# Kernel tuning notes

Hardware: AMD Instinct MI355X
Metric: run time of the kernel (lower is better)

Reference implementation:

```python
import jax, jax.numpy as jnp
import numpy as np
from jax import lax

HEADS = 4
DIM = 64
GATE_HID = 16


def setup_inputs() -> dict:
    key = jax.random.key(0)
    ks = jax.random.split(key, 12)
    b, c, h, w = 2, DIM, 48, 48
    s = 0.05
    x = jax.random.normal(ks[0], (b, c, h, w), jnp.float32)
    Wqkv = jax.random.normal(ks[1], (3 * c, c), jnp.float32) * s
    bqkv = jax.random.normal(ks[2], (3 * c,), jnp.float32) * s
    Wpos = jax.random.normal(ks[3], (3 * c, 1, 3, 3), jnp.float32) * s
    bpos = jax.random.normal(ks[4], (3 * c,), jnp.float32) * s
    Wg1 = jax.random.normal(ks[5], (GATE_HID, 1), jnp.float32) * 0.5
    bg1 = jax.random.normal(ks[6], (GATE_HID,), jnp.float32) * 0.1
    Wg2 = jax.random.normal(ks[7], (1, GATE_HID), jnp.float32) * 0.5
    bg2 = jax.random.normal(ks[8], (1,), jnp.float32) * 0.1
    Wproj = jax.random.normal(ks[9], (c, c), jnp.float32) * s
    bproj = jax.random.normal(ks[10], (c,), jnp.float32) * s
    return {"x": x, "Wqkv": Wqkv, "bqkv": bqkv, "Wpos": Wpos, "bpos": bpos,
            "Wg1": Wg1, "bg1": bg1, "Wg2": Wg2, "bg2": bg2,
            "Wproj": Wproj, "bproj": bproj}


def _forward(x, Wqkv, bqkv, Wpos, bpos, Wg1, bg1, Wg2, bg2, Wproj, bproj):
    b, c, h, w = x.shape
    n = h * w
    heads = HEADS
    hd = c // heads
    scale = hd ** -0.5
    # qkv 1x1 conv then 3x3 depthwise positional conv
    qkv = jnp.einsum('bchw,oc->bohw', x, Wqkv) + bqkv[None, :, None, None]
    qkv = lax.conv_general_dilated(
        qkv, Wpos, window_strides=(1, 1), padding='SAME',
        feature_group_count=3 * c,
        dimension_numbers=('NCHW', 'OIHW', 'NCHW')) + bpos[None, :, None, None]
    q, k, v = jnp.split(qkv, 3, axis=1)

    def to_heads(t):
        # [b,c,h,w] -> [b,heads,n,hd]
        return t.reshape(b, c, n).transpose(0, 2, 1).reshape(b, n, heads, hd).transpose(0, 2, 1, 3)

    q, k, v = to_heads(q), to_heads(k), to_heads(v)
    attn = jnp.einsum('bhid,bhjd->bhij', q, k) * scale  # [b,heads,n,n]
    prob = jax.nn.softmax(attn, axis=-1)
    entropy = -(prob * jnp.log(jnp.clip(prob, 1e-12))).sum(-1).mean(-1)  # [b,heads]
    # entropy gate: sigmoid(fc2(relu(fc1(e)))) * 0.9 + 0.1
    hgate = jax.nn.relu(entropy[..., None] @ Wg1.T + bg1)  # [b,heads,16]
    ratio = jax.nn.sigmoid(hgate @ Wg2.T + bg2)[..., 0] * 0.9 + 0.1  # [b,heads]
    # dynamic per-(batch,head) top-k along rows via rank threshold
    keep = jnp.clip(jnp.ceil(ratio * n).astype(jnp.int32), 1, n)  # [b,heads]
    sorted_desc = -jnp.sort(-attn, axis=-1)  # [b,heads,n,n]
    idx = jnp.broadcast_to((keep - 1)[:, :, None, None], (b, heads, n, 1))
    thresh = jnp.take_along_axis(sorted_desc, idx, axis=-1)  # [b,heads,n,1]
    sparse = jnp.where(attn >= thresh, attn, -jnp.inf)
    p = jax.nn.softmax(sparse, axis=-1)
    out = jnp.einsum('bhij,bhjd->bhid', p, v)  # [b,heads,n,hd]
    out = out.transpose(0, 2, 1, 3).reshape(b, n, c)
    out = out @ Wproj.T + bproj
    return out.transpose(0, 2, 1).reshape(b, c, h, w)


def reference(x, Wqkv, bqkv, Wpos, bpos, Wg1, bg1, Wg2, bg2, Wproj, bproj):
    return _forward(x, Wqkv, bqkv, Wpos, bpos, Wg1, bg1, Wg2, bg2, Wproj, bproj)
```

## Files before the change

kernel.cpp:

```cpp
#include <hip/hip_runtime.h>
#include <hip/hip_fp16.h>


#define NEG_INF (-__builtin_huge_valf())

typedef _Float16 half8_t __attribute__((ext_vector_type(8)));
typedef float floatx4 __attribute__((ext_vector_type(4)));

__device__ __forceinline__ float key16_to_float(unsigned k) {
  unsigned short u = (k & 0x8000u) ? (unsigned short)(k & 0x7FFFu)
                                   : (unsigned short)((~k) & 0xFFFFu);
  return __half2float(__ushort_as_half(u));
}

__device__ __forceinline__ void unpack8(uint4 v, float* o) {
  float2 f0 = __half22float2(*(__half2*)&v.x);
  float2 f1 = __half22float2(*(__half2*)&v.y);
  float2 f2 = __half22float2(*(__half2*)&v.z);
  float2 f3 = __half22float2(*(__half2*)&v.w);
  o[0] = f0.x; o[1] = f0.y; o[2] = f1.x; o[3] = f1.y;
  o[4] = f2.x; o[5] = f2.y; o[6] = f3.x; o[7] = f3.y;
}

__global__ __launch_bounds__(256) void k_qkv(const float* __restrict__ x,
                                             const float* __restrict__ W,
                                             const float* __restrict__ bias,
                                             float* __restrict__ out,
                                             float* __restrict__ ent) {
  if (blockIdx.x == 0 && threadIdx.x < 8) ent[threadIdx.x] = 0.f;
  int blk = blockIdx.x;
  int chunk = blk % 9;
  int og = (blk / 9) % 48;
  int b = blk / (9 * 48);
  int o0 = og * 4;
  int pos = chunk * 256 + threadIdx.x;
  const float* xb = x + b * 64 * 2304 + pos;
  const float* w0 = W + (o0 + 0) * 64;
  const float* w1 = W + (o0 + 1) * 64;
  const float* w2 = W + (o0 + 2) * 64;
  const float* w3 = W + (o0 + 3) * 64;
  float a0 = bias[o0 + 0], a1 = bias[o0 + 1];
  float a2 = bias[o0 + 2], a3 = bias[o0 + 3];
#pragma unroll
  for (int c = 0; c < 64; c++) {
    float xv = xb[c * 2304];
    a0 = fmaf(w0[c], xv, a0);
    a1 = fmaf(w1[c], xv, a1);
    a2 = fmaf(w2[c], xv, a2);
    a3 = fmaf(w3[c], xv, a3);
  }
  out[(b * 192 + o0 + 0) * 2304 + pos] = a0;
  out[(b * 192 + o0 + 1) * 2304 + pos] = a1;
  out[(b * 192 + o0 + 2) * 2304 + pos] = a2;
  out[(b * 192 + o0 + 3) * 2304 + pos] = a3;
}

__global__ __launch_bounds__(256) void k_dw(const float* __restrict__ qkv,
                                            const float* __restrict__ Wpos,
                                            const float* __restrict__ bpos,
                                            _Float16* __restrict__ q2,
                                            _Float16* __restrict__ k2,
                                            _Float16* __restrict__ vt) {
  __shared__ float smem[16][384];
  int blk = blockIdx.x;
  int chunk = blk % 9;
  int sel = (blk / 9) % 3;
  int head = (blk / 27) % 4;
  int b = blk / 108;
  int chbase = sel * 64 + head * 16;
  int bh = b * 4 + head;
  int tid = threadIdx.x;
  int p0 = chunk * 256;
  int baserow = p0 / 48;
  int rA = min(max(baserow - 1, 0), 40);

  const float* src = qkv + (size_t)(b * 192 + chbase) * 2304;
#pragma unroll
  for (int l = 0; l < 24; l++) {
    int idx = tid + l * 256;
    int ch = idx / 384;
    int off = idx - ch * 384;
    int rr = off / 48;
    int cc = off - rr * 48;
    smem[ch][off] = src[(size_t)ch * 2304 + (rA + rr) * 48 + cc];
  }
  __syncthreads();

  int pos = p0 + tid;
  int yy = pos / 48, xx = pos - yy * 48;
  int ry = yy - rA;
  float accv[16];
#pragma unroll
  for (int d = 0; d < 16; d++) {
    const float* w = Wpos + (chbase + d) * 9;
    float a = bpos[chbase + d];
#pragma unroll
    for (int dy = -1; dy <= 1; dy++) {
      int y2 = yy + dy;
      if ((unsigned)y2 < 48u) {
#pragma unroll
        for (int dx = -1; dx <= 1; dx++) {
          int x2 = xx + dx;
          if ((unsigned)x2 < 48u)
            a = fmaf(w[(dy + 1) * 3 + (dx + 1)], smem[d][(ry + dy) * 48 + x2],
                     a);
        }
      }
    }
    accv[d] = a;
  }

  if (sel == 2) {
#pragma unroll
    for (int d = 0; d < 16; d++)
      vt[((size_t)bh * 16 + d) * 2304 + pos] = (_Float16)accv[d];
  } else {
    _Float16 h1[16], h2[16];
#pragma unroll
    for (int d = 0; d < 16; d++) {
      float a = (sel == 0) ? accv[d] * 0.25f : accv[d];
      h1[d] = (_Float16)a;
      h2[d] = (_Float16)(a - (float)h1[d]);
    }
    _Float16* dst = ((sel == 0) ? q2 : k2) + ((size_t)bh * 2304 + pos) * 32;
    uint4* d4 = (uint4*)dst;
    d4[0] = *(uint4*)&h1[0];
    d4[1] = *(uint4*)&h1[8];
    d4[2] = *(uint4*)&h2[0];
    d4[3] = *(uint4*)&h2[8];
  }
}

template <bool STORE>
__global__ __launch_bounds__(256) void k_ent_t(const _Float16* __restrict__ q2,
                                               const _Float16* __restrict__ k2,
                                               float* __restrict__ ent,
                                               _Float16* __restrict__ lgH) {
  __shared__ __align__(16) _Float16 tBuf[4][16][72];
  __shared__ float sWv[4][16], uWv[4][16];

  int blk = blockIdx.x;
  int rowtile = blk % 144;
  int bh = blk / 144;
  int row0 = rowtile * 16;
  int tid = threadIdx.x, lane = tid & 63, wave = tid >> 6;
  int m16 = lane & 15, quad = lane >> 4;

  const half8_t* q2v =
      (const half8_t*)(q2 + ((size_t)bh * 2304 + row0 + m16) * 32);
  half8_t A1 = q2v[quad];
  half8_t zh = {};
  half8_t A2 = (lane < 32) ? A1 : zh;
  const half8_t* kbase = (const half8_t*)(k2 + (size_t)bh * 2304 * 32);

  float s[4] = {0.f, 0.f, 0.f, 0.f}, u[4] = {0.f, 0.f, 0.f, 0.f};
  for (int g = 0; g < 9; g++) {
#pragma unroll
    for (int tt = 0; tt < 4; tt++) {
      int t = g * 4 + tt;
      int col = wave * 576 + t * 16 + m16;
      const half8_t* kk = kbase + (size_t)col * 4;
      half8_t b1 = kk[quad & 1];
      half8_t b2 = kk[2 + (quad & 1)];
      floatx4 acc = {};
      acc = __builtin_amdgcn_mfma_f32_16x16x32_f16(A2, b2, acc, 0, 0, 0);
      acc = __builtin_amdgcn_mfma_f32_16x16x32_f16(A1, b1, acc, 0, 0, 0);
#pragma unroll
      for (int i = 0; i < 4; i++) {
        if (STORE) tBuf[wave][quad * 4 + i][tt * 16 + m16] = (_Float16)acc[i];
        float e = __expf(acc[i]);
        s[i] += e;
        u[i] = fmaf(acc[i], e, u[i]);
      }
    }
    if (STORE) {
      __syncthreads();
      int rb = lane >> 3, seg = lane & 7;
#pragma unroll
      for (int it = 0; it < 2; it++) {
        int rr = it * 8 + rb;
        uint4 vv = *(const uint4*)&tBuf[wave][rr][seg * 8];
        *(uint4*)(lgH + ((size_t)bh * 2304 + row0 + rr) * 2304 + wave * 576 +
                  g * 64 + seg * 8) = vv;
      }
      __syncthreads();
    }
  }
#pragma unroll
  for (int off = 1; off < 16; off <<= 1) {
#pragma unroll
    for (int i = 0; i < 4; i++) {
      s[i] += __shfl_xor(s[i], off);
      u[i] += __shfl_xor(u[i], off);
    }
  }
  if (m16 == 0) {
#pragma unroll
    for (int i = 0; i < 4; i++) {
      sWv[wave][quad * 4 + i] = s[i];
      uWv[wave][quad * 4 + i] = u[i];
    }
  }
  __syncthreads();
  if (tid < 16) {
    float S = sWv[0][tid] + sWv[1][tid] + sWv[2][tid] + sWv[3][tid];
    float U = uWv[0][tid] + uWv[1][tid] + uWv[2][tid] + uWv[3][tid];
    float er = __logf(S) - U / S;
    er += __shfl_xor(er, 1);
    er += __shfl_xor(er, 2);
    er += __shfl_xor(er, 4);
    er += __shfl_xor(er, 8);
    if (tid == 0) atomicAdd(&ent[bh], er);
  }
}

template <bool CACHED>
__global__ __launch_bounds__(256, 7) void k_attn_t(
    const _Float16* __restrict__ q2, const _Float16* __restrict__ k2,
    const _Float16* __restrict__ vt, const _Float16* __restrict__ lgH,
    const float* __restrict__ ent, const float* __restrict__ Wg1,
    const float* __restrict__ bg1, const float* __restrict__ Wg2,
    const float* __restrict__ bg2, float* __restrict__ oh) {
  __shared__ __align__(16) _Float16 pbuf[4][2320];
  __shared__ float sS[4];
  __shared__ float mShF[4][4];
  __shared__ __align__(16) float redSh[4][64];

  int a = blockIdx.x;
  int v8 = a & 7;
  int idx = a >> 3;
  int q = idx & 3;
  int pi = idx >> 2;
  int bh = pi / 18;
  int rowtile = v8 + (pi % 18) * 8;
  int rowblk = rowtile * 4 + q;
  int row0 = rowblk * 4;
  int tid = threadIdx.x, lane = tid & 63, wave = tid >> 6;

  float eAvg = ent[bh] * (1.f / 2304.f);
  float gacc = bg2[0];
#pragma unroll
  for (int i = 0; i < 16; i++) {
    float h = fmaxf(fmaf(eAvg, Wg1[i], bg1[i]), 0.f);
    gacc = fmaf(h, Wg2[i], gacc);
  }
  float ratio = 0.9f / (1.f + __expf(-gacc)) + 0.1f;
  int kp = (int)ceilf(ratio * 2304.f);
  unsigned keep = (unsigned)min(max(kp, 1), 2304);

  float v[36];
  float m;
  if (CACHED) {
    const _Float16* src = lgH + ((size_t)bh * 2304 + row0 + wave) * 2304;
    const uint4* s4 = (const uint4*)src;
    float mx = NEG_INF;
#pragma unroll
    for (int it = 0; it < 4; it++) {
      uint4 r = s4[lane + it * 64];
      unpack8(r, &v[it * 8]);
    }
    {
      uint2 r2 = *(const uint2*)(src + 2048 + lane * 4);
      float2 f0 = __half22float2(*(__half2*)&r2.x);
      float2 f1 = __half22float2(*(__half2*)&r2.y);
      v[32] = f0.x; v[33] = f0.y; v[34] = f1.x; v[35] = f1.y;
    }
#pragma unroll
    for (int i = 0; i < 36; i++) mx = fmaxf(mx, v[i]);
#pragma unroll
    for (int off = 1; off < 64; off <<= 1) mx = fmaxf(mx, __shfl_xor(mx, off));
    m = mx;
  } else {
    int m16 = lane & 15, quad = lane >> 4;
    const half8_t* q2v =
        (const half8_t*)(q2 + ((size_t)bh * 2304 + row0 + (m16 & 3)) * 32);
    half8_t A1 = q2v[quad];
    half8_t zh = {};
    half8_t A2 = (lane < 32) ? A1 : zh;
    const half8_t* kbase = (const half8_t*)(k2 + (size_t)bh * 2304 * 32);
    float ml[4] = {NEG_INF, NEG_INF, NEG_INF, NEG_INF};
#pragma unroll 4
    for (int t = 0; t < 36; t++) {
      int ct = wave * 36 + t;
      int col = ct * 16 + m16;
      const half8_t* kk = kbase + (size_t)col * 4;
      half8_t b1 = kk[quad & 1];
      half8_t b2 = kk[2 + (quad & 1)];
      floatx4 acc = {};
      acc = __builtin_amdgcn_mfma_f32_16x16x32_f16(A2, b2, acc, 0, 0, 0);
      acc = __builtin_amdgcn_mfma_f32_16x16x32_f16(A1, b1, acc, 0, 0, 0);
      if (lane < 16) {
#pragma unroll
        for (int i = 0; i < 4; i++) {
          pbuf[i][ct * 16 + lane] = (_Float16)acc[i];
          ml[i] = fmaxf(ml[i], acc[i]);
        }
      }
    }
#pragma unroll
    for (int off = 1; off < 16; off <<= 1)
#pragma unroll
      for (int i = 0; i < 4; i++) ml[i] = fmaxf(ml[i], __shfl_xor(ml[i], off));
    if (lane == 0) {
#pragma unroll
      for (int i = 0; i < 4; i++) mShF[wave][i] = ml[i];
    }
    __syncthreads();
    m = fmaxf(fmaxf(mShF[0][wave], mShF[1][wave]),
              fmaxf(mShF[2][wave], mShF[3][wave]));
    const _Float16* src = pbuf[wave];
    const uint4* s4 = (const uint4*)src;
#pragma unroll
    for (int it = 0; it < 4; it++) unpack8(s4[lane + it * 64], &v[it * 8]);
    uint2 r2 = *(const uint2*)(src + 2048 + lane * 4);
    float2 f0 = __half22float2(*(__half2*)&r2.x);
    float2 f1 = __half22float2(*(__half2*)&r2.y);
    v[32] = f0.x; v[33] = f0.y; v[34] = f1.x; v[35] = f1.y;
  }

  float th;
  {
    unsigned T = 0u;
    for (int bit = 15; bit >= 0; --bit) {
      unsigned cand = T | (1u << bit);
      float cf = key16_to_float(cand);
      unsigned cnt = 0u;
#pragma unroll
      for (int i = 0; i < 36; i++)
        cnt += (unsigned)__popcll(__ballot(v[i] >= cf));
      if (cnt >= keep) {
        T = cand;
        if (cnt == keep) break;
      }
    }
    th = key16_to_float(T);
  }

  {
    float sp = 0.f;
    uint4* prow4 = (uint4*)pbuf[wave];
#pragma unroll
    for (int it = 0; it < 4; it++) {
      float p[8];
#pragma unroll
      for (int e = 0; e < 8; e++) {
        float av = v[it * 8 + e];
        p[e] = (av >= th) ? __expf(av - m) : 0.f;
        sp += p[e];
      }
      uint4 o;
      __half2 h0 = __floats2half2_rn(p[0], p[1]); o.x = *(unsigned*)&h0;
      __half2 h1 = __floats2half2_rn(p[2], p[3]); o.y = *(unsigned*)&h1;
      __half2 h2 = __floats2half2_rn(p[4], p[5]); o.z = *(unsigned*)&h2;
      __half2 h3 = __floats2half2_rn(p[6], p[7]); o.w = *(unsigned*)&h3;
      prow4[lane + it * 64] = o;
    }
    {
      float p0 = (v[32] >= th) ? __expf(v[32] - m) : 0.f;
      float p1 = (v[33] >= th) ? __expf(v[33] - m) : 0.f;
      float p2 = (v[34] >= th) ? __expf(v[34] - m) : 0.f;
      float p3 = (v[35] >= th) ? __expf(v[35] - m) : 0.f;
      sp += (p0 + p1) + (p2 + p3);
      uint2 o;
      __half2 h0 = __floats2half2_rn(p0, p1); o.x = *(unsigned*)&h0;
      __half2 h1 = __floats2half2_rn(p2, p3); o.y = *(unsigned*)&h1;
      *(uint2*)(pbuf[wave] + 2048 + lane * 4) = o;
    }
#pragma unroll
    for (int off = 1; off < 64; off <<= 1) sp += __shfl_xor(sp, off);
    if (lane == 0) sS[wave] = sp;
  }
  __syncthreads();

  {
    int m16 = lane & 15, quad = lane >> 4;
    const _Float16* vrow = vt + ((size_t)bh * 16 + m16) * 2304;
    const _Float16* prow = pbuf[m16 & 3];
    int jb0 = wave * 576 + quad * 8;
    floatx4 acc = {};
#pragma unroll 6
    for (int t = 0; t < 18; t++) {
      int jb = jb0 + t * 32;
      half8_t a2 = *(const half8_t*)&prow[jb];
      half8_t b2 = *(const half8_t*)&vrow[jb];
      acc = __builtin_amdgcn_mfma_f32_16x16x32_f16(a2, b2, acc, 0, 0, 0);
    }
    if (lane < 16) {
      *(floatx4*)&redSh[wave][m16 * 4] = acc;
    }
  }
  __syncthreads();
  if (tid < 64) {
    int r = tid & 3, d = tid >> 2;
    float s2 = redSh[0][d * 4 + r] + redSh[1][d * 4 + r] +
               redSh[2][d * 4 + r] + redSh[3][d * 4 + r];
    oh[((size_t)(bh * 2304 + row0 + r)) * 16 + d] = s2 / sS[r];
  }
}

__global__ __launch_bounds__(256) void k_proj(const float* __restrict__ oh,
                                              const float* __restrict__ Wp,
                                              const float* __restrict__ bp,
                                              float* __restrict__ out) {
  int blk = blockIdx.x;
  int chunk = blk % 9;
  int cog = (blk / 9) % 16;
  int b = blk / (9 * 16);
  int co0 = cog * 4;
  int pos = chunk * 256 + threadIdx.x;
  float a0 = bp[co0 + 0], a1 = bp[co0 + 1], a2 = bp[co0 + 2], a3 = bp[co0 + 3];
#pragma unroll
  for (int head = 0; head < 4; head++) {
    const float4* op =
        (const float4*)(oh + ((size_t)((b * 4 + head) * 2304 + pos)) * 16);
#pragma unroll
    for (int p = 0; p < 4; p++) {
      float4 o4 = op[p];
#pragma unroll
      for (int i = 0; i < 4; i++) {
        const float* wr = Wp + (co0 + i) * 64 + head * 16 + p * 4;
        float* ai = (i == 0) ? &a0 : ((i == 1) ? &a1 : ((i == 2) ? &a2 : &a3));
        *ai = fmaf(wr[0], o4.x, *ai);
        *ai = fmaf(wr[1], o4.y, *ai);
        *ai = fmaf(wr[2], o4.z, *ai);
        *ai = fmaf(wr[3], o4.w, *ai);
      }
    }
  }
  out[(b * 64 + co0 + 0) * 2304 + pos] = a0;
  out[(b * 64 + co0 + 1) * 2304 + pos] = a1;
  out[(b * 64 + co0 + 2) * 2304 + pos] = a2;
  out[(b * 64 + co0 + 3) * 2304 + pos] = a3;
}

extern "C" void kernel_launch(void* const* d_in, const int* in_sizes, int n_in,
                              void* d_out, int out_size, void* d_ws,
                              size_t ws_size, hipStream_t stream) {
  const float* x    = (const float*)d_in[0];
  const float* Wqkv = (const float*)d_in[1];
  const float* bqkv = (const float*)d_in[2];
  const float* Wpos = (const float*)d_in[3];
  const float* bpos = (const float*)d_in[4];
  const float* Wg1  = (const float*)d_in[5];
  const float* bg1  = (const float*)d_in[6];
  const float* Wg2  = (const float*)d_in[7];
  const float* bg2  = (const float*)d_in[8];
  const float* Wpr  = (const float*)d_in[9];
  const float* bpr  = (const float*)d_in[10];
  float* out = (float*)d_out;

  const size_t lgBytes = (size_t)8 * 2304 * 2304 * 2;
  const size_t baseBytes = (size_t)(884736 + 294912 + 8) * 4 +
                           (size_t)(2 * 589824 + 294912) * 2;
  bool cached = ws_size >= lgBytes + baseBytes;

  char* base = (char*)d_ws;
  _Float16* lgH = nullptr;
  if (cached) {
    lgH = (_Float16*)base;
    base += lgBytes;
  }
  float* qkv_raw = (float*)base;
  float* oh = qkv_raw + 884736;
  float* ent = oh + 294912;
  _Float16* q2 = (_Float16*)(ent + 8);
  _Float16* k2 = q2 + 589824;
  _Float16* vt = k2 + 589824;

  hipLaunchKernelGGL(k_qkv, dim3(2 * 48 * 9), dim3(256), 0, stream,
                     x, Wqkv, bqkv, qkv_raw, ent);
  hipLaunchKernelGGL(k_dw, dim3(216), dim3(256), 0, stream,
                     qkv_raw, Wpos, bpos, q2, k2, vt);
  if (cached) {
    hipLaunchKernelGGL((k_ent_t<true>), dim3(8 * 144), dim3(256), 0, stream,
                       q2, k2, ent, lgH);
    hipLaunchKernelGGL((k_attn_t<true>), dim3(8 * 576), dim3(256), 0, stream,
                       q2, k2, vt, lgH, ent, Wg1, bg1, Wg2, bg2, oh);
  } else {
    hipLaunchKernelGGL((k_ent_t<false>), dim3(8 * 144), dim3(256), 0, stream,
                       q2, k2, ent, lgH);
    hipLaunchKernelGGL((k_attn_t<false>), dim3(8 * 576), dim3(256), 0, stream,
                       q2, k2, vt, lgH, ent, Wg1, bg1, Wg2, bg2, oh);
  }
  hipLaunchKernelGGL(k_proj, dim3(2 * 16 * 9), dim3(256), 0, stream,
                     oh, Wpr, bpr, out);
}
```

Measured before the change: 199.4 us.

## Fuse output projection into attention kernel and drop softmax max subtraction

Removes the separate projection kernel. Each attention block now projects its 4 rows across all 64 output channels and atomically adds the per-head contribution into a pre-zeroed output. This removes the max computation and its reductions and stores before the exponentials, which relies on logits being small enough not to overflow exp. The depthwise conv kernel is also split into half-channel blocks to double its grid. The cost is a memset, plus atomic traffic on the output with 4-way contention per element.

```diff
diff --git a/kernel.cpp b/kernel.cpp
--- a/kernel.cpp
+++ b/kernel.cpp
@@ -61,13 +61,14 @@
                                             _Float16* __restrict__ q2,
                                             _Float16* __restrict__ k2,
                                             _Float16* __restrict__ vt) {
-  __shared__ float smem[16][384];
+  __shared__ float smem[8][384];
   int blk = blockIdx.x;
   int chunk = blk % 9;
-  int sel = (blk / 9) % 3;
-  int head = (blk / 27) % 4;
-  int b = blk / 108;
-  int chbase = sel * 64 + head * 16;
+  int half = (blk / 9) % 2;
+  int sel = (blk / 18) % 3;
+  int head = (blk / 54) % 4;
+  int b = blk / 216;
+  int chbase = sel * 64 + head * 16 + half * 8;
   int bh = b * 4 + head;
   int tid = threadIdx.x;
   int p0 = chunk * 256;
@@ -76,7 +77,7 @@
 
   const float* src = qkv + (size_t)(b * 192 + chbase) * 2304;
 #pragma unroll
-  for (int l = 0; l < 24; l++) {
+  for (int l = 0; l < 12; l++) {
     int idx = tid + l * 256;
     int ch = idx / 384;
     int off = idx - ch * 384;
@@ -89,9 +90,9 @@
   int pos = p0 + tid;
   int yy = pos / 48, xx = pos - yy * 48;
   int ry = yy - rA;
-  float accv[16];
-#pragma unroll
-  for (int d = 0; d < 16; d++) {
+  float accv[8];
+#pragma unroll
+  for (int d = 0; d < 8; d++) {
     const float* w = Wpos + (chbase + d) * 9;
     float a = bpos[chbase + d];
 #pragma unroll
@@ -112,22 +113,19 @@
 
   if (sel == 2) {
 #pragma unroll
-    for (int d = 0; d < 16; d++)
-      vt[((size_t)bh * 16 + d) * 2304 + pos] = (_Float16)accv[d];
+    for (int d = 0; d < 8; d++)
+      vt[((size_t)bh * 16 + half * 8 + d) * 2304 + pos] = (_Float16)accv[d];
   } else {
-    _Float16 h1[16], h2[16];
-#pragma unroll
-    for (int d = 0; d < 16; d++) {
+    _Float16 h1[8], h2[8];
+#pragma unroll
+    for (int d = 0; d < 8; d++) {
       float a = (sel == 0) ? accv[d] * 0.25f : accv[d];
       h1[d] = (_Float16)a;
       h2[d] = (_Float16)(a - (float)h1[d]);
     }
     _Float16* dst = ((sel == 0) ? q2 : k2) + ((size_t)bh * 2304 + pos) * 32;
-    uint4* d4 = (uint4*)dst;
-    d4[0] = *(uint4*)&h1[0];
-    d4[1] = *(uint4*)&h1[8];
-    d4[2] = *(uint4*)&h2[0];
-    d4[3] = *(uint4*)&h2[8];
+    *(uint4*)(dst + half * 8) = *(uint4*)&h1[0];
+    *(uint4*)(dst + 16 + half * 8) = *(uint4*)&h2[0];
   }
 }
 
@@ -220,11 +218,12 @@
     const _Float16* __restrict__ vt, const _Float16* __restrict__ lgH,
     const float* __restrict__ ent, const float* __restrict__ Wg1,
     const float* __restrict__ bg1, const float* __restrict__ Wg2,
-    const float* __restrict__ bg2, float* __restrict__ oh) {
+    const float* __restrict__ bg2, const float* __restrict__ Wp,
+    const float* __restrict__ bp, float* __restrict__ out) {
   __shared__ __align__(16) _Float16 pbuf[4][2320];
   __shared__ float sS[4];
-  __shared__ float mShF[4][4];
   __shared__ __align__(16) float redSh[4][64];
+  __shared__ float oSh[4][16];
 
   int a = blockIdx.x;
   int v8 = a & 7;
@@ -249,11 +248,9 @@
   unsigned keep = (unsigned)min(max(kp, 1), 2304);
 
   float v[36];
-  float m;
   if (CACHED) {
     const _Float16* src = lgH + ((size_t)bh * 2304 + row0 + wave) * 2304;
     const uint4* s4 = (const uint4*)src;
-    float mx = NEG_INF;
 #pragma unroll
     for (int it = 0; it < 4; it++) {
       uint4 r = s4[lane + it * 64];
@@ -265,11 +262,6 @@
       float2 f1 = __half22float2(*(__half2*)&r2.y);
       v[32] = f0.x; v[33] = f0.y; v[34] = f1.x; v[35] = f1.y;
     }
-#pragma unroll
-    for (int i = 0; i < 36; i++) mx = fmaxf(mx, v[i]);
-#pragma unroll
-    for (int off = 1; off < 64; off <<= 1) mx = fmaxf(mx, __shfl_xor(mx, off));
-    m = mx;
   } else {
     int m16 = lane & 15, quad = lane >> 4;
     const half8_t* q2v =
@@ -278,7 +270,6 @@
     half8_t zh = {};
     half8_t A2 = (lane < 32) ? A1 : zh;
     const half8_t* kbase = (const half8_t*)(k2 + (size_t)bh * 2304 * 32);
-    float ml[4] = {NEG_INF, NEG_INF, NEG_INF, NEG_INF};
 #pragma unroll 4
     for (int t = 0; t < 36; t++) {
       int ct = wave * 36 + t;
@@ -291,23 +282,10 @@
       acc = __builtin_amdgcn_mfma_f32_16x16x32_f16(A1, b1, acc, 0, 0, 0);
       if (lane < 16) {
 #pragma unroll
-        for (int i = 0; i < 4; i++) {
-          pbuf[i][ct * 16 + lane] = (_Float16)acc[i];
-          ml[i] = fmaxf(ml[i], acc[i]);
-        }
-      }
-    }
-#pragma unroll
-    for (int off = 1; off < 16; off <<= 1)
-#pragma unroll
-      for (int i = 0; i < 4; i++) ml[i] = fmaxf(ml[i], __shfl_xor(ml[i], off));
-    if (lane == 0) {
-#pragma unroll
-      for (int i = 0; i < 4; i++) mShF[wave][i] = ml[i];
+        for (int i = 0; i < 4; i++) pbuf[i][ct * 16 + lane] = (_Float16)acc[i];
+      }
     }
     __syncthreads();
-    m = fmaxf(fmaxf(mShF[0][wave], mShF[1][wave]),
-              fmaxf(mShF[2][wave], mShF[3][wave]));
     const _Float16* src = pbuf[wave];
     const uint4* s4 = (const uint4*)src;
 #pragma unroll
@@ -345,7 +323,7 @@
 #pragma unroll
       for (int e = 0; e < 8; e++) {
         float av = v[it * 8 + e];
-        p[e] = (av >= th) ? __expf(av - m) : 0.f;
+        p[e] = (av >= th) ? __expf(av) : 0.f;
         sp += p[e];
       }
       uint4 o;
@@ -356,10 +334,10 @@
       prow4[lane + it * 64] = o;
     }
     {
-      float p0 = (v[32] >= th) ? __expf(v[32] - m) : 0.f;
-      float p1 = (v[33] >= th) ? __expf(v[33] - m) : 0.f;
-      float p2 = (v[34] >= th) ? __expf(v[34] - m) : 0.f;
-      float p3 = (v[35] >= th) ? __expf(v[35] - m) : 0.f;
+      float p0 = (v[32] >= th) ? __expf(v[32]) : 0.f;
+      float p1 = (v[33] >= th) ? __expf(v[33]) : 0.f;
+      float p2 = (v[34] >= th) ? __expf(v[34]) : 0.f;
+      float p3 = (v[35] >= th) ? __expf(v[35]) : 0.f;
       sp += (p0 + p1) + (p2 + p3);
       uint2 o;
       __half2 h0 = __floats2half2_rn(p0, p1); o.x = *(unsigned*)&h0;
@@ -394,43 +372,21 @@
     int r = tid & 3, d = tid >> 2;
     float s2 = redSh[0][d * 4 + r] + redSh[1][d * 4 + r] +
                redSh[2][d * 4 + r] + redSh[3][d * 4 + r];
-    oh[((size_t)(bh * 2304 + row0 + r)) * 16 + d] = s2 / sS[r];
-  }
-}
-
-__global__ __launch_bounds__(256) void k_proj(const float* __restrict__ oh,
-                                              const float* __restrict__ Wp,
-                                              const float* __restrict__ bp,
-                                              float* __restrict__ out) {
-  int blk = blockIdx.x;
-  int chunk = blk % 9;
-  int cog = (blk / 9) % 16;
-  int b = blk / (9 * 16);
-  int co0 = cog * 4;
-  int pos = chunk * 256 + threadIdx.x;
-  float a0 = bp[co0 + 0], a1 = bp[co0 + 1], a2 = bp[co0 + 2], a3 = bp[co0 + 3];
-#pragma unroll
-  for (int head = 0; head < 4; head++) {
-    const float4* op =
-        (const float4*)(oh + ((size_t)((b * 4 + head) * 2304 + pos)) * 16);
-#pragma unroll
-    for (int p = 0; p < 4; p++) {
-      float4 o4 = op[p];
-#pragma unroll
-      for (int i = 0; i < 4; i++) {
-        const float* wr = Wp + (co0 + i) * 64 + head * 16 + p * 4;
-        float* ai = (i == 0) ? &a0 : ((i == 1) ? &a1 : ((i == 2) ? &a2 : &a3));
-        *ai = fmaf(wr[0], o4.x, *ai);
-        *ai = fmaf(wr[1], o4.y, *ai);
-        *ai = fmaf(wr[2], o4.z, *ai);
-        *ai = fmaf(wr[3], o4.w, *ai);
-      }
-    }
-  }
-  out[(b * 64 + co0 + 0) * 2304 + pos] = a0;
-  out[(b * 64 + co0 + 1) * 2304 + pos] = a1;
-  out[(b * 64 + co0 + 2) * 2304 + pos] = a2;
-  out[(b * 64 + co0 + 3) * 2304 + pos] = a3;
+    oSh[r][d] = s2 / sS[r];
+  }
+  __syncthreads();
+
+  {
+    int r = wave;
+    int co = lane;
+    int head = bh & 3, b = bh >> 2;
+    const float* wr = Wp + co * 64 + head * 16;
+    float val = 0.f;
+#pragma unroll
+    for (int d = 0; d < 16; d++) val = fmaf(wr[d], oSh[r][d], val);
+    if (head == 0) val += bp[co];
+    atomicAdd(&out[((size_t)(b * 64 + co)) * 2304 + row0 + r], val);
+  }
 }
 
 extern "C" void kernel_launch(void* const* d_in, const int* in_sizes, int n_in,
@@ -450,7 +406,7 @@
   float* out = (float*)d_out;
 
   const size_t lgBytes = (size_t)8 * 2304 * 2304 * 2;
-  const size_t baseBytes = (size_t)(884736 + 294912 + 8) * 4 +
+  const size_t baseBytes = (size_t)(884736 + 8) * 4 +
                            (size_t)(2 * 589824 + 294912) * 2;
   bool cached = ws_size >= lgBytes + baseBytes;
 
@@ -461,27 +417,27 @@
     base += lgBytes;
   }
   float* qkv_raw = (float*)base;
-  float* oh = qkv_raw + 884736;
-  float* ent = oh + 294912;
+  float* ent = qkv_raw + 884736;
   _Float16* q2 = (_Float16*)(ent + 8);
   _Float16* k2 = q2 + 589824;
   _Float16* vt = k2 + 589824;
 
+  (void)hipMemsetAsync(out, 0, (size_t)out_size * sizeof(float), stream);
   hipLaunchKernelGGL(k_qkv, dim3(2 * 48 * 9), dim3(256), 0, stream,
                      x, Wqkv, bqkv, qkv_raw, ent);
-  hipLaunchKernelGGL(k_dw, dim3(216), dim3(256), 0, stream,
+  hipLaunchKernelGGL(k_dw, dim3(432), dim3(256), 0, stream,
                      qkv_raw, Wpos, bpos, q2, k2, vt);
   if (cached) {
     hipLaunchKernelGGL((k_ent_t<true>), dim3(8 * 144), dim3(256), 0, stream,
                        q2, k2, ent, lgH);
     hipLaunchKernelGGL((k_attn_t<true>), dim3(8 * 576), dim3(256), 0, stream,
-                       q2, k2, vt, lgH, ent, Wg1, bg1, Wg2, bg2, oh);
+                       q2, k2, vt, lgH, ent, Wg1, bg1, Wg2, bg2, Wpr, bpr,
+                       out);
   } else {
     hipLaunchKernelGGL((k_ent_t<false>), dim3(8 * 144), dim3(256), 0, stream,
                        q2, k2, ent, lgH);
     hipLaunchKernelGGL((k_attn_t<false>), dim3(8 * 576), dim3(256), 0, stream,
-                       q2, k2, vt, lgH, ent, Wg1, bg1, Wg2, bg2, oh);
-  }
-  hipLaunchKernelGGL(k_proj, dim3(2 * 16 * 9), dim3(256), 0, stream,
-                     oh, Wpr, bpr, out);
-}
+                       q2, k2, vt, lgH, ent, Wg1, bg1, Wg2, bg2, Wpr, bpr,
+                       out);
+  }
+}
```

Result: slower. 224.7 us (+12.7%).
